# Kernel tuning notes

Hardware: AMD Instinct MI355X
Metric: run time of the kernel (lower is better)

Reference implementation:

```python
import jax, jax.numpy as jnp
import numpy as np

HID = 5120       # hidden_size
H = 32           # num_heads (TP shard)
Q_RANK = 1536    # q_lora_rank
KV_RANK = 512    # kv_lora_rank
D_NOPE = 128     # qk_nope_head_dim
D_ROPE = 64      # qk_rope_head_dim
DV = 128         # v_head_dim
Q_HEAD = D_NOPE + D_ROPE
T = 2048
EPS = 1e-6
ROPE_BASE = 10000.0
SCALE = Q_HEAD ** -0.5
NEG = jnp.finfo(jnp.float32).min


def rmsnorm(x, w):
    return x * jax.lax.rsqrt(jnp.mean(x * x, axis=-1, keepdims=True) + EPS) * w


def rope(x, pos):
    # half-split (GPT-NeoX style) rotary; the torch module permutes weights in
    # _update_pe so that interleaved RoPE becomes exactly this half-split form.
    half = x.shape[-1] // 2
    inv = 1.0 / (ROPE_BASE ** (jnp.arange(half, dtype=jnp.float32) / half))
    ang = pos.astype(jnp.float32)[:, None] * inv          # [T, half]
    cos, sin = jnp.cos(ang), jnp.sin(ang)
    if x.ndim == 3:                                       # [T, H, D]
        cos, sin = cos[:, None, :], sin[:, None, :]
    x1, x2 = jnp.split(x, 2, axis=-1)
    return jnp.concatenate([x1 * cos - x2 * sin, x2 * cos + x1 * sin], axis=-1)


def setup_inputs() -> dict:
    key = jax.random.key(0)
    ks = jax.random.split(key, 10)
    s = 0.02
    return {
        'hidden_states': jax.random.normal(ks[0], (1, T, HID), jnp.float32),
        'position_ids': jnp.arange(T, dtype=jnp.int64),
        'w_q_a': jax.random.normal(ks[1], (Q_RANK, HID), jnp.float32) * s,
        'q_a_ln_w': jnp.ones((Q_RANK,), jnp.float32),
        'w_q_b': jax.random.normal(ks[2], (H * Q_HEAD, Q_RANK), jnp.float32) * s,
        'w_kv_a': jax.random.normal(ks[3], (KV_RANK + D_ROPE, HID), jnp.float32) * s,
        'kv_a_ln_w': jnp.ones((KV_RANK,), jnp.float32),
        'w_kc': jax.random.normal(ks[4], (H, D_NOPE, KV_RANK), jnp.float32) * s,
        'w_vc': jax.random.normal(ks[5], (H, KV_RANK, DV), jnp.float32) * s,
        'w_o': jax.random.normal(ks[6], (HID, H * DV), jnp.float32) * s,
    }


def reference(hidden_states, position_ids, w_q_a, q_a_ln_w, w_q_b, w_kv_a,
              kv_a_ln_w, w_kc, w_vc, w_o):
    h = hidden_states[0]                                   # [T, HID]
    t = h.shape[0]
    # q low-rank path: q_a_proj -> rmsnorm -> q_b_proj
    q = rmsnorm(h @ w_q_a.T, q_a_ln_w) @ w_q_b.T           # [T, H*Q_HEAD]
    q = q.reshape(t, H, Q_HEAD)
    q_nope, q_pe = q[..., :D_NOPE], q[..., D_NOPE:]
    # absorb kv_b (w_kc): project q into the latent kv space
    q_lat = jnp.einsum('thn,hnk->thk', q_nope, w_kc)       # [T, H, KV_RANK]
    # kv low-rank path (MQA-style shared latent)
    ckv_full = h @ w_kv_a.T                                # [T, KV_RANK+D_ROPE]
    ckv = rmsnorm(ckv_full[:, :KV_RANK], kv_a_ln_w)        # [T, KV_RANK]
    k_pe = rope(ckv_full[:, KV_RANK:], position_ids)       # [T, D_ROPE]
    q_pe = rope(q_pe, position_ids)                        # [T, H, D_ROPE]
    # full query/key in latent+pe space; key/value shared across heads
    qf = jnp.concatenate([q_lat, q_pe], axis=-1)           # [T, H, KV_RANK+D_ROPE]
    kf = jnp.concatenate([ckv, k_pe], axis=-1)             # [T, KV_RANK+D_ROPE]
    scores = jnp.einsum('thd,sd->hts', qf, kf) * SCALE     # [H, T, T]
    causal = jnp.tril(jnp.ones((t, t), dtype=bool))
    scores = jnp.where(causal[None], scores, NEG)
    p = jax.nn.softmax(scores, axis=-1)
    o = jnp.einsum('hts,sk->thk', p, ckv)                  # [T, H, KV_RANK]
    o = jnp.einsum('thk,hkv->thv', o, w_vc)                # [T, H, DV]
    out = o.reshape(t, H * DV) @ w_o.T                     # [T, HID]
    return out[None]
```

## Files before the change

### kernel.cpp

```cpp
#include <hip/hip_runtime.h>
#include <hip/hip_bf16.h>
#include <type_traits>

typedef __attribute__((ext_vector_type(8))) short short8;
typedef __attribute__((ext_vector_type(4))) float f32x4;
using bf16 = __hip_bfloat16;

#define T_SEQ 2048
#define NH 32
#define SCALE_F 0.07216878364870323f

__device__ inline unsigned short f2bf(float f) {
    unsigned u = __builtin_bit_cast(unsigned, f);
    return (unsigned short)((u + 0x7fffu + ((u >> 16) & 1u)) >> 16);
}

__device__ inline void gload_lds16(const void* g, void* l) {
    __builtin_amdgcn_global_load_lds(
        (const __attribute__((address_space(1))) unsigned*)g,
        (__attribute__((address_space(3))) unsigned*)l, 16, 0, 0);
}

template <typename TC>
__global__ __launch_bounds__(256, 2) void gemmhw_kernel(
    const bf16* __restrict__ A, const bf16* __restrict__ B, TC* __restrict__ C,
    int K, int lda, int ldb, int ldc,
    long aStride, long bStride, long cStride)
{
    const int z = blockIdx.z;
    A += (long)z * aStride; B += (long)z * bStride; C += (long)z * cStride;
    const int bm = blockIdx.y * 256, bn = blockIdx.x * 128;
    __shared__ __align__(16) short As[2][256 * 32];
    __shared__ __align__(16) short Bs[2][128 * 32];
    const int tid = threadIdx.x, lane = tid & 63, w = tid >> 6;
    const int l15 = lane & 15, lg = lane >> 4;
    const int wm = w >> 1, wn = w & 1;
    const int sx = (lane & 7) ^ (lane >> 3);
    const int lrh = lane >> 3;
    const int srp = sx >> 2;
    const int scol = (sx & 3) * 8;
    const bf16* Ab = A + (long)bm * lda;
    const bf16* Bb = B + (long)bn * ldb;

    auto stage = [&](int buf, int k0) {
        #pragma unroll
        for (int jj = 0; jj < 4; ++jj) {
            const int j = w * 4 + jj;
            const int srow = 2 * (j * 8 + lrh) + srp;
            gload_lds16(Ab + (long)srow * lda + k0 + scol, &As[buf][j * 512]);
        }
        #pragma unroll
        for (int jj = 0; jj < 2; ++jj) {
            const int j = w * 2 + jj;
            const int srow = 2 * (j * 8 + lrh) + srp;
            gload_lds16(Bb + (long)srow * ldb + k0 + scol, &Bs[buf][j * 512]);
        }
    };

    const int rslot = ((((l15 & 1) << 2) | lg) ^ (l15 >> 1)) << 4;
    const int lrow_lo = l15 >> 1;
    f32x4 acc[8][4] = {};
    const int nt = K >> 5;
    stage(0, 0);
    for (int t = 0; t < nt; ++t) {
        if (t + 1 < nt) {
            stage((t + 1) & 1, (t + 1) << 5);
            asm volatile("s_waitcnt vmcnt(6)" ::: "memory");
        } else {
            asm volatile("s_waitcnt vmcnt(0)" ::: "memory");
        }
        __builtin_amdgcn_s_barrier();
        __builtin_amdgcn_sched_barrier(0);
        const char* Ap = (const char*)&As[t & 1][0];
        const char* Bp = (const char*)&Bs[t & 1][0];
        short8 af[8], bf[4];
        #pragma unroll
        for (int fi = 0; fi < 8; ++fi)
            af[fi] = *(const short8*)(Ap + (wm * 64 + fi * 8 + lrow_lo) * 128 + rslot);
        #pragma unroll
        for (int nj = 0; nj < 4; ++nj)
            bf[nj] = *(const short8*)(Bp + (wn * 32 + nj * 8 + lrow_lo) * 128 + rslot);
        #pragma unroll
        for (int fi = 0; fi < 8; ++fi)
            #pragma unroll
            for (int nj = 0; nj < 4; ++nj)
                acc[fi][nj] = __builtin_amdgcn_mfma_f32_16x16x32_bf16(
                    af[fi], bf[nj], acc[fi][nj], 0, 0, 0);
        asm volatile("s_waitcnt lgkmcnt(0)" ::: "memory");
        __builtin_amdgcn_sched_barrier(0);
        __builtin_amdgcn_s_barrier();
        __builtin_amdgcn_sched_barrier(0);
    }
    #pragma unroll
    for (int fi = 0; fi < 8; ++fi)
        #pragma unroll
        for (int nj = 0; nj < 4; ++nj)
            #pragma unroll
            for (int i = 0; i < 4; ++i) {
                const int row = bm + wm * 128 + fi * 16 + lg * 4 + i;
                const int col = bn + wn * 64 + nj * 16 + l15;
                if constexpr (std::is_same<TC, float>::value)
                    C[(long)row * ldc + col] = acc[fi][nj][i];
                else
                    ((unsigned short*)C)[(long)row * ldc + col] = f2bf(acc[fi][nj][i]);
            }
}

template <typename TC>
__global__ __launch_bounds__(512, 4) void gemm8w_kernel(
    const bf16* __restrict__ A, const bf16* __restrict__ B, TC* __restrict__ C,
    int K, int lda, int ldb, int ldc,
    long aStride, long bStride, long cStride)
{
    const int z = blockIdx.z;
    A += (long)z * aStride; B += (long)z * bStride; C += (long)z * cStride;
    const int bm = blockIdx.y * 128, bn = blockIdx.x * 128;
    __shared__ __align__(16) short As[2][128 * 64];
    __shared__ __align__(16) short Bs[2][128 * 64];
    const int tid = threadIdx.x, lane = tid & 63, w = tid >> 6;
    const int l15 = lane & 15, lg = lane >> 4;
    const int wm = w >> 1, wn = w & 1;
    const int c0 = w * 2, c1 = w * 2 + 1;
    const int srow0 = c0 * 8 + (lane >> 3), srow1 = c1 * 8 + (lane >> 3);
    const int scol = ((lane & 7) * 16) ^ ((lane >> 3) << 4);
    const bf16* Ab = A + (long)bm * lda;
    const bf16* Bb = B + (long)bn * ldb;

    auto stage = [&](int buf, int k0) {
        const char* ag = (const char*)(Ab + k0);
        const char* bg = (const char*)(Bb + k0);
        gload_lds16(ag + (long)srow0 * (lda * 2) + scol, &As[buf][c0 * 512]);
        gload_lds16(ag + (long)srow1 * (lda * 2) + scol, &As[buf][c1 * 512]);
        gload_lds16(bg + (long)srow0 * (ldb * 2) + scol, &Bs[buf][c0 * 512]);
        gload_lds16(bg + (long)srow1 * (ldb * 2) + scol, &Bs[buf][c1 * 512]);
    };

    const int swz = (l15 & 7) << 4;
    f32x4 acc[2][4] = {};
    const int nt = K >> 6;
    stage(0, 0);
    for (int t = 0; t < nt; ++t) {
        if (t + 1 < nt) {
            stage((t + 1) & 1, (t + 1) << 6);
            asm volatile("s_waitcnt vmcnt(4)" ::: "memory");
        } else {
            asm volatile("s_waitcnt vmcnt(0)" ::: "memory");
        }
        __builtin_amdgcn_s_barrier();
        __builtin_amdgcn_sched_barrier(0);
        const char* Ap = (const char*)&As[t & 1][0];
        const char* Bp = (const char*)&Bs[t & 1][0];
        short8 af[2][2], bfv[4][2];
        #pragma unroll
        for (int fi = 0; fi < 2; ++fi)
            #pragma unroll
            for (int ks = 0; ks < 2; ++ks)
                af[fi][ks] = *(const short8*)(Ap + (wm * 32 + fi * 16 + l15) * 128
                                              + ((ks * 64 + lg * 16) ^ swz));
        #pragma unroll
        for (int nj = 0; nj < 4; ++nj)
            #pragma unroll
            for (int ks = 0; ks < 2; ++ks)
                bfv[nj][ks] = *(const short8*)(Bp + (wn * 64 + nj * 16 + l15) * 128
                                               + ((ks * 64 + lg * 16) ^ swz));
        #pragma unroll
        for (int ks = 0; ks < 2; ++ks)
            #pragma unroll
            for (int fi = 0; fi < 2; ++fi)
                #pragma unroll
                for (int nj = 0; nj < 4; ++nj)
                    acc[fi][nj] = __builtin_amdgcn_mfma_f32_16x16x32_bf16(
                        af[fi][ks], bfv[nj][ks], acc[fi][nj], 0, 0, 0);
        asm volatile("s_waitcnt lgkmcnt(0)" ::: "memory");
        __builtin_amdgcn_sched_barrier(0);
        __builtin_amdgcn_s_barrier();
        __builtin_amdgcn_sched_barrier(0);
    }
    #pragma unroll
    for (int fi = 0; fi < 2; ++fi)
        #pragma unroll
        for (int nj = 0; nj < 4; ++nj)
            #pragma unroll
            for (int i = 0; i < 4; ++i) {
                const int row = bm + wm * 32 + fi * 16 + lg * 4 + i;
                const int col = bn + wn * 64 + nj * 16 + l15;
                if constexpr (std::is_same<TC, float>::value)
                    C[(long)row * ldc + col] = acc[fi][nj][i];
                else
                    ((unsigned short*)C)[(long)row * ldc + col] = f2bf(acc[fi][nj][i]);
            }
}

__global__ __launch_bounds__(256) void cvt_kernel(
    const float* __restrict__ in, bf16* __restrict__ out, long n, float scale)
{
    const long i = ((long)blockIdx.x * 256 + threadIdx.x) * 8;
    if (i >= n) return;
    f32x4 a = *(const f32x4*)(in + i), b = *(const f32x4*)(in + i + 4);
    short8 r;
    r[0] = (short)f2bf(a[0] * scale); r[1] = (short)f2bf(a[1] * scale);
    r[2] = (short)f2bf(a[2] * scale); r[3] = (short)f2bf(a[3] * scale);
    r[4] = (short)f2bf(b[0] * scale); r[5] = (short)f2bf(b[1] * scale);
    r[6] = (short)f2bf(b[2] * scale); r[7] = (short)f2bf(b[3] * scale);
    *(short8*)(out + i) = r;
}

__global__ __launch_bounds__(256) void tconv_kernel(
    const float* __restrict__ in, bf16* __restrict__ out)
{
    const int h = blockIdx.z, k0 = blockIdx.x * 32, d0 = blockIdx.y * 32;
    __shared__ float t[32][33];
    const int r = threadIdx.x >> 5, c = threadIdx.x & 31;
    const float* ip = in + ((long)h * 512 + k0) * 128 + d0;
    #pragma unroll
    for (int it = 0; it < 4; ++it)
        t[r + 8 * it][c] = ip[(long)(r + 8 * it) * 128 + c];
    __syncthreads();
    bf16* op = out + ((long)h * 128 + d0) * 512 + k0;
    #pragma unroll
    for (int it = 0; it < 4; ++it)
        op[(long)(r + 8 * it) * 512 + c] = __float2bfloat16(t[c][r + 8 * it]);
}

__global__ __launch_bounds__(256) void rmsnorm_kernel(
    bf16* __restrict__ x, const float* __restrict__ w, int C, int ld)
{
    bf16* row = x + (long)blockIdx.x * ld;
    float ss = 0.f;
    for (int i = threadIdx.x; i < C; i += 256) {
        float v = __bfloat162float(row[i]);
        ss += v * v;
    }
    #pragma unroll
    for (int m = 1; m < 64; m <<= 1) ss += __shfl_xor(ss, m, 64);
    __shared__ float red[4];
    if ((threadIdx.x & 63) == 0) red[threadIdx.x >> 6] = ss;
    __syncthreads();
    ss = red[0] + red[1] + red[2] + red[3];
    float scale = rsqrtf(ss / (float)C + 1e-6f);
    for (int i = threadIdx.x; i < C; i += 256) {
        float v = __bfloat162float(row[i]);
        row[i] = __float2bfloat16(v * scale * w[i]);
    }
}

__global__ __launch_bounds__(256) void ropeq_kernel(bf16* __restrict__ q)
{
    const int t = blockIdx.x;
    #pragma unroll
    for (int it = 0; it < 4; ++it) {
        const int pair = threadIdx.x + 256 * it;
        const int h = pair >> 5, i = pair & 31;
        bf16* base = q + ((long)t * NH + h) * 192;
        float x1 = __bfloat162float(base[128 + i]);
        float x2 = __bfloat162float(base[160 + i]);
        float inv = powf(10000.f, -(float)i / 32.f);
        float ang = (float)t * inv, s, c;
        sincosf(ang, &s, &c);
        base[128 + i] = __float2bfloat16(x1 * c - x2 * s);
        base[160 + i] = __float2bfloat16(x2 * c + x1 * s);
    }
}

__global__ __launch_bounds__(1024) void ropek_kernel(
    const bf16* __restrict__ ckv, bf16* __restrict__ kf, int ld)
{
    const int t = blockIdx.x;
    const int h = threadIdx.x >> 5, i = threadIdx.x & 31;
    float x1 = __bfloat162float(ckv[(long)t * ld + 512 + i]);
    float x2 = __bfloat162float(ckv[(long)t * ld + 544 + i]);
    float inv = powf(10000.f, -(float)i / 32.f);
    float ang = (float)t * inv, s, c;
    sincosf(ang, &s, &c);
    bf16* kb = kf + ((long)h * T_SEQ + t) * 192;
    kb[128 + i] = __float2bfloat16(x1 * c - x2 * s);
    kb[160 + i] = __float2bfloat16(x2 * c + x1 * s);
}

__global__ __launch_bounds__(256, 2) void attn_kernel(
    const bf16* __restrict__ Q,
    const bf16* __restrict__ Kf,
    const bf16* __restrict__ Vt,
    bf16* __restrict__ O)
{
    const int lin = blockIdx.x;
    const int h = (lin & 7) + 8 * ((lin >> 3) & 3);
    const int qraw = lin >> 5;
    const int qblk = (qraw < 8) ? (2 * qraw) : (31 - 2 * qraw);
    const int q0 = qblk * 128;
    const int tid = threadIdx.x, lane = tid & 63, w = tid >> 6;
    const int l15 = lane & 15, lg = lane >> 4;
    const int qw = q0 + w * 32;
    __shared__ __align__(16) short Ks[64 * 192];
    __shared__ __align__(16) short Vs[128 * 64];

    int ksoff[6];
    #pragma unroll
    for (int j = 0; j < 6; ++j) {
        int o = (w * 6 + j) * 1024 + lane * 16;
        int row = o / 384, col = o % 384;
        ksoff[j] = row * 384 + (col ^ ((row & 7) << 4));
    }
    const int vrow8 = lane >> 3;
    const int vscol = ((lane & 7) * 16) ^ (vrow8 << 4);

    short8 qf[2][6];
    #pragma unroll
    for (int qi = 0; qi < 2; ++qi) {
        const bf16* qp = Q + (long)(qw + qi * 16 + l15) * (NH * 192) + (long)h * 192;
        #pragma unroll
        for (int c = 0; c < 6; ++c) qf[qi][c] = *(const short8*)(qp + c * 32 + lg * 8);
    }

    f32x4 oacc[2][8] = {};
    float mst[2] = {-INFINITY, -INFINITY};
    float lst[2] = {0.f, 0.f};

    const char* kbase0 = (const char*)Kf + (long)h * T_SEQ * 384;
    const char* vbase0 = (const char*)Vt + (long)h * 128 * (T_SEQ * 2);
    const int swz = (l15 & 7) << 4;

    for (int s0 = 0; s0 < q0 + 128; s0 += 64) {
        {
            const char* kb = kbase0 + (long)s0 * 384;
            #pragma unroll
            for (int j = 0; j < 6; ++j)
                gload_lds16(kb + ksoff[j], (char*)Ks + (w * 6 + j) * 1024);
            const char* vb = vbase0 + (long)s0 * 2 + vscol;
            #pragma unroll
            for (int j = 0; j < 4; ++j) {
                const int c = w * 4 + j;
                gload_lds16(vb + (long)(c * 8 + vrow8) * (T_SEQ * 2),
                            (char*)Vs + c * 1024);
            }
        }
        __syncthreads();
        if (s0 <= qw + 31) {
            f32x4 st[2][4] = {};
            __builtin_amdgcn_s_setprio(1);
            #pragma unroll
            for (int cb = 0; cb < 4; ++cb) {
                const int krow = cb * 16 + l15;
                #pragma unroll
                for (int c = 0; c < 6; ++c) {
                    short8 kfr = *(const short8*)((const char*)Ks + krow * 384
                                                  + ((c * 64 + lg * 16) ^ swz));
                    st[0][cb] = __builtin_amdgcn_mfma_f32_16x16x32_bf16(kfr, qf[0][c], st[0][cb], 0, 0, 0);
                    st[1][cb] = __builtin_amdgcn_mfma_f32_16x16x32_bf16(kfr, qf[1][c], st[1][cb], 0, 0, 0);
                }
            }
            __builtin_amdgcn_s_setprio(0);
            short8 pb[2][2];
            #pragma unroll
            for (int qi = 0; qi < 2; ++qi) {
                const int qg = qw + qi * 16 + l15;
                float pmax = -INFINITY;
                #pragma unroll
                for (int cb = 0; cb < 4; ++cb)
                    #pragma unroll
                    for (int i = 0; i < 4; ++i) {
                        const int kv = s0 + cb * 16 + lg * 4 + i;
                        float v = (kv <= qg) ? st[qi][cb][i] : -INFINITY;
                        st[qi][cb][i] = v;
                        pmax = fmaxf(pmax, v);
                    }
                pmax = fmaxf(pmax, __shfl_xor(pmax, 16, 64));
                pmax = fmaxf(pmax, __shfl_xor(pmax, 32, 64));
                const float newm = fmaxf(mst[qi], pmax);
                const float mm = (newm == -INFINITY) ? 0.f : newm;
                const float alpha = __expf(mst[qi] - mm);
                float ps = 0.f;
                #pragma unroll
                for (int cb = 0; cb < 4; ++cb)
                    #pragma unroll
                    for (int i = 0; i < 4; ++i) {
                        const float e = __expf(st[qi][cb][i] - mm);
                        st[qi][cb][i] = e; ps += e;
                    }
                ps += __shfl_xor(ps, 16, 64);
                ps += __shfl_xor(ps, 32, 64);
                lst[qi] = lst[qi] * alpha + ps;
                mst[qi] = newm;
                #pragma unroll
                for (int mb = 0; mb < 8; ++mb) oacc[qi][mb] *= alpha;
                #pragma unroll
                for (int hh = 0; hh < 2; ++hh) {
                    unsigned pk[4];
                    #pragma unroll
                    for (int i = 0; i < 4; ++i)
                        pk[i] = (unsigned)f2bf(st[qi][2 * hh][i])
                              | ((unsigned)f2bf(st[qi][2 * hh + 1][i]) << 16);
                    #pragma unroll
                    for (int j = 0; j < 8; ++j) {
                        const int src = l15 + (((2 * lg + (j >> 2)) & 3) << 4);
                        const unsigned u = (unsigned)__shfl((int)pk[j & 3], src, 64);
                        pb[qi][hh][j] = (short)((lg >> 1) ? (u >> 16) : (u & 0xffffu));
                    }
                }
            }
            __builtin_amdgcn_s_setprio(1);
            #pragma unroll
            for (int mb = 0; mb < 8; ++mb) {
                const int vrow = mb * 16 + l15;
                #pragma unroll
                for (int hh = 0; hh < 2; ++hh) {
                    short8 vfr = *(const short8*)((const char*)Vs + vrow * 128
                                                  + ((hh * 64 + lg * 16) ^ swz));
                    oacc[0][mb] = __builtin_amdgcn_mfma_f32_16x16x32_bf16(vfr, pb[0][hh], oacc[0][mb], 0, 0, 0);
                    oacc[1][mb] = __builtin_amdgcn_mfma_f32_16x16x32_bf16(vfr, pb[1][hh], oacc[1][mb], 0, 0, 0);
                }
            }
            __builtin_amdgcn_s_setprio(0);
        }
        __syncthreads();
    }
    #pragma unroll
    for (int qi = 0; qi < 2; ++qi) {
        const float inv = 1.f / lst[qi];
        const int qg = qw + qi * 16 + l15;
        #pragma unroll
        for (int mb = 0; mb < 8; ++mb)
            #pragma unroll
            for (int i = 0; i < 4; ++i) {
                const int dv = mb * 16 + lg * 4 + i;
                O[(long)qg * (NH * 128) + h * 128 + dv] = __float2bfloat16(oacc[qi][mb][i] * inv);
            }
    }
}

extern "C" void kernel_launch(void* const* d_in, const int* in_sizes, int n_in,
                              void* d_out, int out_size, void* d_ws, size_t ws_size,
                              hipStream_t stream)
{
    const float* hidden    = (const float*)d_in[0];
    const float* w_q_a     = (const float*)d_in[2];
    const float* q_a_ln_w  = (const float*)d_in[3];
    const float* w_q_b     = (const float*)d_in[4];
    const float* w_kv_a    = (const float*)d_in[5];
    const float* kv_a_ln_w = (const float*)d_in[6];
    const float* w_kc      = (const float*)d_in[7];
    const float* w_vc      = (const float*)d_in[8];
    const float* w_o       = (const float*)d_in[9];
    float* out = (float*)d_out;

    bf16* qckv  = (bf16*)d_ws;
    bf16* qbuf  = qckv  + (long)T_SEQ * 2176;
    bf16* kf    = qbuf  + (long)T_SEQ * 6144;
    bf16* vt    = kf    + (long)NH * T_SEQ * 192;
    bf16* ov    = vt    + (long)NH * 128 * T_SEQ;
    bf16* hb    = ov    + (long)T_SEQ * 4096;
    bf16* wqckv = hb    + (long)T_SEQ * 5120;
    bf16* wqb   = wqckv + (long)2176 * 5120;
    bf16* wkc   = wqb   + (long)6144 * 1536;
    bf16* wvct  = wkc   + (long)NH * 128 * 512;
    bf16* wo    = hb;
    bf16* ckv   = qckv + 1536;

    cvt_kernel<<<dim3(5120), 256, 0, stream>>>(hidden, hb, (long)T_SEQ * 5120, 1.f);
    cvt_kernel<<<dim3(3840), 256, 0, stream>>>(w_q_a, wqckv, (long)1536 * 5120, 1.f);
    cvt_kernel<<<dim3(1440), 256, 0, stream>>>(w_kv_a, wqckv + (long)1536 * 5120,
                                               (long)576 * 5120, 1.f);
    hipMemsetAsync(wqckv + (long)2112 * 5120, 0, (long)64 * 5120 * sizeof(bf16), stream);
    cvt_kernel<<<dim3(4608), 256, 0, stream>>>(w_q_b, wqb, (long)6144 * 1536, SCALE_F);
    cvt_kernel<<<dim3(1024), 256, 0, stream>>>(w_kc, wkc, (long)NH * 128 * 512, 1.f);
    tconv_kernel<<<dim3(16, 4, NH), 256, 0, stream>>>(w_vc, wvct);

    gemm8w_kernel<bf16><<<dim3(17, 16, 1), 512, 0, stream>>>(
        hb, wqckv, qckv, 5120, 5120, 5120, 2176, 0, 0, 0);
    rmsnorm_kernel<<<dim3(T_SEQ), 256, 0, stream>>>(qckv, q_a_ln_w, 1536, 2176);
    rmsnorm_kernel<<<dim3(T_SEQ), 256, 0, stream>>>(ckv, kv_a_ln_w, 512, 2176);
    gemmhw_kernel<bf16><<<dim3(48, 8, 1), 256, 0, stream>>>(
        qckv, wqb, qbuf, 1536, 2176, 1536, 6144, 0, 0, 0);
    ropeq_kernel<<<dim3(T_SEQ), 256, 0, stream>>>(qbuf);
    ropek_kernel<<<dim3(T_SEQ), 1024, 0, stream>>>(ckv, kf, 2176);
    gemmhw_kernel<bf16><<<dim3(1, 8, NH), 256, 0, stream>>>(
        ckv, wkc, kf, 512, 2176, 512, 192,
        0, (long)128 * 512, (long)T_SEQ * 192);
    gemm8w_kernel<bf16><<<dim3(16, 1, NH), 512, 0, stream>>>(
        wvct, ckv, vt, 512, 512, 2176, T_SEQ,
        (long)128 * 512, 0, (long)128 * T_SEQ);
    cvt_kernel<<<dim3(10240), 256, 0, stream>>>(w_o, wo, (long)5120 * 4096, 1.f);
    attn_kernel<<<dim3(512), 256, 0, stream>>>(qbuf, kf, vt, ov);
    gemmhw_kernel<float><<<dim3(40, 8, 1), 256, 0, stream>>>(
        ov, wo, out, 4096, 4096, 4096, 5120, 0, 0, 0);
}
```

Before: 496.3 us.

## Add 256x256-tile 8-wave ping-pong GEMM for q_b and output projections

Adds a new 512-thread GEMM kernel with 256x256 output tiles, 64-wide K steps, double-buffered 128KB dynamic LDS, and swizzled direct global-to-LDS loads. Each K step is split into four quadrant MFMA phases, with half-tile staging interleaved between them and setprio raised around the MFMA bursts. The kernel replaces the 256x128 gemmhw for the q_b projection and the final output projection to raise arithmetic intensity and overlap loads with MFMA work. Larger tiles mean fewer blocks (192 and 160), which may underfill the GPU's CUs. The 128KB LDS allocation also limits occupancy.

```diff
diff --git a/kernel.cpp b/kernel.cpp
--- a/kernel.cpp
+++ b/kernel.cpp
@@ -19,6 +19,119 @@
     __builtin_amdgcn_global_load_lds(
         (const __attribute__((address_space(1))) unsigned*)g,
         (__attribute__((address_space(3))) unsigned*)l, 16, 0, 0);
+}
+
+template <typename TC>
+__global__ __launch_bounds__(512, 2) void gemm8p_kernel(
+    const bf16* __restrict__ A, const bf16* __restrict__ B, TC* __restrict__ C,
+    int K, int lda, int ldb, int ldc)
+{
+    extern __shared__ char Lds[];
+    const int bm = blockIdx.y * 256, bn = blockIdx.x * 256;
+    const int tid = threadIdx.x, lane = tid & 63, w = tid >> 6;
+    const int l15 = lane & 15, lg = lane >> 4;
+    const int wmr = (w >> 2) * 64;
+    const int wnc = (w & 3) * 32;
+    const int lrh = lane >> 3;
+    const int scolb = ((lane & 7) * 16) ^ ((lane >> 3) << 4);
+    const int rdswz = (l15 & 7) << 4;
+    const bf16* Ab = A + (long)bm * lda;
+    const bf16* Bb = B + (long)bn * ldb;
+    const int nt = K >> 6;
+
+    auto stage_half = [&](int tt, int isB, int h) {
+        const int buf = tt & 1;
+        const int k0 = (tt >= nt ? tt - nt : tt) << 6;
+        const bf16* Base = isB ? Bb : Ab;
+        const int ld = isB ? ldb : lda;
+        const char* g = (const char*)Base
+            + ((long)(h * 128 + w * 8 + lrh) * ld + k0) * 2 + scolb;
+        char* l = Lds + buf * 65536 + isB * 32768 + h * 16384 + w * 1024;
+        gload_lds16(g, l);
+        gload_lds16(g + (long)128 * ld, l + 8192);
+    };
+
+    f32x4 acc[4][4][2] = {};
+    stage_half(0, 0, 0); stage_half(0, 1, 1); stage_half(0, 0, 1);
+    stage_half(0, 1, 0); stage_half(1, 0, 0); stage_half(1, 1, 1);
+    asm volatile("s_waitcnt vmcnt(4)" ::: "memory");
+    __builtin_amdgcn_s_barrier();
+
+    for (int t = 0; t < nt; ++t) {
+        const char* Bufp = Lds + (t & 1) * 65536;
+        short8 aF[4][2], bF[2][2];
+        #define ARD(mh, fi, ks) \
+            (*(const short8*)(Bufp + (mh) * 16384 + (wmr + (fi) * 16 + l15) * 128 \
+                              + (((ks) * 64 + lg * 16) ^ rdswz)))
+        #define BRD(nh, nj, ks) \
+            (*(const short8*)(Bufp + 32768 + (nh) * 16384 + (wnc + (nj) * 16 + l15) * 128 \
+                              + (((ks) * 64 + lg * 16) ^ rdswz)))
+        #define MFMA16(q) \
+            __builtin_amdgcn_s_setprio(1); \
+            _Pragma("unroll") for (int ks = 0; ks < 2; ++ks) \
+            _Pragma("unroll") for (int fi = 0; fi < 4; ++fi) \
+            _Pragma("unroll") for (int nj = 0; nj < 2; ++nj) \
+                acc[q][fi][nj] = __builtin_amdgcn_mfma_f32_16x16x32_bf16( \
+                    aF[fi][ks], bF[nj][ks], acc[q][fi][nj], 0, 0, 0); \
+            __builtin_amdgcn_s_setprio(0);
+
+        #pragma unroll
+        for (int fi = 0; fi < 4; ++fi) { aF[fi][0] = ARD(0, fi, 0); aF[fi][1] = ARD(0, fi, 1); }
+        #pragma unroll
+        for (int nj = 0; nj < 2; ++nj) { bF[nj][0] = BRD(0, nj, 0); bF[nj][1] = BRD(0, nj, 1); }
+        stage_half(t + 1, 0, 1);
+        asm volatile("s_waitcnt lgkmcnt(8)" ::: "memory");
+        __builtin_amdgcn_s_barrier();
+        asm volatile("s_waitcnt lgkmcnt(0)" ::: "memory");
+        __builtin_amdgcn_sched_barrier(0);
+        MFMA16(0)
+        __builtin_amdgcn_s_barrier();
+        #pragma unroll
+        for (int nj = 0; nj < 2; ++nj) { bF[nj][0] = BRD(1, nj, 0); bF[nj][1] = BRD(1, nj, 1); }
+        stage_half(t + 1, 1, 0);
+        __builtin_amdgcn_s_barrier();
+        asm volatile("s_waitcnt lgkmcnt(0)" ::: "memory");
+        __builtin_amdgcn_sched_barrier(0);
+        MFMA16(1)
+        __builtin_amdgcn_s_barrier();
+        #pragma unroll
+        for (int fi = 0; fi < 4; ++fi) { aF[fi][0] = ARD(1, fi, 0); aF[fi][1] = ARD(1, fi, 1); }
+        stage_half(t + 2, 0, 0);
+        __builtin_amdgcn_s_barrier();
+        asm volatile("s_waitcnt lgkmcnt(0)" ::: "memory");
+        __builtin_amdgcn_sched_barrier(0);
+        MFMA16(2)
+        __builtin_amdgcn_s_barrier();
+        #pragma unroll
+        for (int nj = 0; nj < 2; ++nj) { bF[nj][0] = BRD(0, nj, 0); bF[nj][1] = BRD(0, nj, 1); }
+        stage_half(t + 2, 1, 1);
+        __builtin_amdgcn_s_barrier();
+        asm volatile("s_waitcnt lgkmcnt(0)" ::: "memory");
+        __builtin_amdgcn_sched_barrier(0);
+        MFMA16(3)
+        asm volatile("s_waitcnt vmcnt(4)" ::: "memory");
+        __builtin_amdgcn_s_barrier();
+        #undef ARD
+        #undef BRD
+        #undef MFMA16
+    }
+    asm volatile("s_waitcnt vmcnt(0)" ::: "memory");
+    const int QMH[4] = {0, 0, 1, 1}, QNH[4] = {0, 1, 1, 0};
+    #pragma unroll
+    for (int q = 0; q < 4; ++q)
+        #pragma unroll
+        for (int fi = 0; fi < 4; ++fi)
+            #pragma unroll
+            for (int nj = 0; nj < 2; ++nj)
+                #pragma unroll
+                for (int i = 0; i < 4; ++i) {
+                    const int row = bm + QMH[q] * 128 + wmr + fi * 16 + lg * 4 + i;
+                    const int col = bn + QNH[q] * 128 + wnc + nj * 16 + l15;
+                    if constexpr (std::is_same<TC, float>::value)
+                        C[(long)row * ldc + col] = acc[q][fi][nj][i];
+                    else
+                        ((unsigned short*)C)[(long)row * ldc + col] = f2bf(acc[q][fi][nj][i]);
+                }
 }
 
 template <typename TC>
@@ -469,8 +582,8 @@
         hb, wqckv, qckv, 5120, 5120, 5120, 2176, 0, 0, 0);
     rmsnorm_kernel<<<dim3(T_SEQ), 256, 0, stream>>>(qckv, q_a_ln_w, 1536, 2176);
     rmsnorm_kernel<<<dim3(T_SEQ), 256, 0, stream>>>(ckv, kv_a_ln_w, 512, 2176);
-    gemmhw_kernel<bf16><<<dim3(48, 8, 1), 256, 0, stream>>>(
-        qckv, wqb, qbuf, 1536, 2176, 1536, 6144, 0, 0, 0);
+    gemm8p_kernel<bf16><<<dim3(24, 8), 512, 131072, stream>>>(
+        qckv, wqb, qbuf, 1536, 2176, 1536, 6144);
     ropeq_kernel<<<dim3(T_SEQ), 256, 0, stream>>>(qbuf);
     ropek_kernel<<<dim3(T_SEQ), 1024, 0, stream>>>(ckv, kf, 2176);
     gemmhw_kernel<bf16><<<dim3(1, 8, NH), 256, 0, stream>>>(
@@ -481,6 +594,6 @@
         (long)128 * 512, 0, (long)128 * T_SEQ);
     cvt_kernel<<<dim3(10240), 256, 0, stream>>>(w_o, wo, (long)5120 * 4096, 1.f);
     attn_kernel<<<dim3(512), 256, 0, stream>>>(qbuf, kf, vt, ov);
-    gemmhw_kernel<float><<<dim3(40, 8, 1), 256, 0, stream>>>(
-        ov, wo, out, 4096, 4096, 4096, 5120, 0, 0, 0);
-}
+    gemm8p_kernel<float><<<dim3(20, 8), 512, 131072, stream>>>(
+        ov, wo, out, 4096, 4096, 4096, 5120);
+}
```

Measured after the change: 465.9 us. -6.1%, faster.
